# Optimization experiments

Hardware: AMD Instinct MI355X
Metric: run time of the kernel (lower is better)

The kernel has to match this reference:

```python
import jax, jax.numpy as jnp
import numpy as np

HOURS = 168  # 24*7
SU, SL, TU, TL = 100.0, 0.0, 500.0, 0.0  # ex bounds
N, M, L, D, T = 64, 128, 8192, 64, 169  # batch, max_len, l_dim(=u_dim), d_model, t_dim


def setup_inputs() -> dict:
    key = jax.random.key(0)
    ks = jax.random.split(key, 20)
    traj = jax.random.randint(ks[0], (N, M, 3), 1, L)          # [user, loc, time] indices, >=1
    mat1 = jax.random.uniform(ks[1], (N, M, M, 2), jnp.float32) * jnp.asarray([SU, TU], jnp.float32)
    mat2s = jax.random.uniform(ks[2], (L, L), jnp.float32) * SU
    vec = jax.random.uniform(ks[3], (N, M), jnp.float32) * TU
    traj_len = jax.random.randint(ks[4], (N,), 1, M + 1)
    s = 0.02
    emb_t = (jax.random.normal(ks[5], (T, D), jnp.float32) * s).at[0].set(0.0)
    emb_l = (jax.random.normal(ks[6], (L, D), jnp.float32) * s).at[0].set(0.0)
    emb_u = (jax.random.normal(ks[7], (L, D), jnp.float32) * s).at[0].set(0.0)
    emb_su = (jax.random.normal(ks[8], (2, D), jnp.float32) * s).at[0].set(0.0)
    emb_sl = (jax.random.normal(ks[9], (2, D), jnp.float32) * s).at[0].set(0.0)
    emb_tu = (jax.random.normal(ks[10], (2, D), jnp.float32) * s).at[0].set(0.0)
    emb_tl = (jax.random.normal(ks[11], (2, D), jnp.float32) * s).at[0].set(0.0)
    Wq = jax.random.normal(ks[12], (D, D), jnp.float32) * s
    Wk = jax.random.normal(ks[13], (D, D), jnp.float32) * s
    Wv = jax.random.normal(ks[14], (D, D), jnp.float32) * s
    W_out = jax.random.normal(ks[15], (L, D), jnp.float32) * s
    b_out = jnp.zeros((L,), jnp.float32)
    return dict(traj=traj, mat1=mat1, mat2s=mat2s, vec=vec, traj_len=traj_len,
                emb_t=emb_t, emb_l=emb_l, emb_u=emb_u, emb_su=emb_su, emb_sl=emb_sl,
                emb_tu=emb_tu, emb_tl=emb_tl, Wq=Wq, Wk=Wk, Wv=Wv, W_out=W_out, b_out=b_out)


def reference(traj, mat1, mat2s, vec, traj_len, emb_t, emb_l, emb_u,
              emb_su, emb_sl, emb_tu, emb_tl, Wq, Wk, Wv, W_out, b_out):
    # ---- MultiEmbed ----
    time_idx = (traj[:, :, 2] - 1) % HOURS + 1
    joint = emb_t[time_idx] + emb_l[traj[:, :, 1]] + emb_u[traj[:, :, 0]]  # (N,M,D)
    ds, dt = mat1[..., 0], mat1[..., 1]                                    # (N,M,M)
    valid = jnp.arange(M)[None, :] < traj_len[:, None]                     # (N,M)
    mask2 = (valid[:, :, None] & valid[:, None, :]).astype(jnp.int32)      # (N,M,M)
    # delta is only consumed as delta.sum(-1) in SelfAttn; sum over emb dim
    # factors out since vsl/vsu/vtl/vtu are constant over emb -> (N,M,M) only.
    ssl, ssu = emb_sl.sum(-1), emb_su.sum(-1)  # (2,)
    stl, stu = emb_tl.sum(-1), emb_tu.sum(-1)
    delta_sum = ((ssl[mask2] * (SU - ds) + ssu[mask2] * (ds - SL)) / (SU - SL)
                 + (stl[mask2] * (TU - dt) + stu[mask2] * (dt - TL)) / (TU - TL))  # (N,M,M)
    # ---- SelfAttn ----
    q = joint @ Wq.T
    k = joint @ Wk.T
    v = joint @ Wv.T
    scores = jnp.einsum('nmd,npd->nmp', q, k) + delta_sum
    attn = jax.nn.softmax(scores, axis=-1) * mask2.astype(jnp.float32)  # post-softmax ragged mask
    self_attn = jnp.einsum('nmp,npd->nmd', attn, v)                     # (N,M,D)
    # ---- Embed: self_delta (N,M,L,D) consumed only as sum over L in Attn ----
    # mask there equals valid[n,m] for every candidate l, and delta_t = vec for all l,
    # so sum over L collapses to per-(n,m) scalars.
    m1 = valid.astype(jnp.int32)                                  # (N,M)
    E_sl, E_su = emb_sl[m1], emb_su[m1]                           # (N,M,D)
    E_tl, E_tu = emb_tl[m1], emb_tu[m1]
    ds_sum = jnp.where(valid, mat2s.sum(-1)[traj[:, :, 1] - 1], 0.0)  # sum_l delta_s (N,M)
    Lf = jnp.float32(L)
    S_vsl = ds_sum - SL * Lf
    S_vsu = SU * Lf - ds_sum
    S_vtl = (vec - TL) * Lf
    S_vtu = (TU - vec) * Lf
    delta2_sum = ((E_sl * S_vsu[..., None] + E_su * S_vsl[..., None]) / (SU - SL)
                  + (E_tl * S_vtu[..., None] + E_tu * S_vtl[..., None]) / (TU - TL))  # (N,M,D)
    # ---- Attn (training branch: return full logits) ----
    out = (self_attn * delta2_sum) @ W_out.T + b_out  # (N,M,L)
    return out
```

## Files before the change

### kernel.cpp

```cpp
#include <hip/hip_runtime.h>
#include <stdint.h>

#define NB 64
#define MM 128
#define LL 8192
#define DD 64

using f32x4 = __attribute__((ext_vector_type(4))) float;
using bf16x8 = __attribute__((ext_vector_type(8))) short;

__device__ __forceinline__ float bf2f(uint32_t u16) {
    uint32_t v = u16 << 16;
    float f;
    __builtin_memcpy(&f, &v, 4);
    return f;
}
__device__ __forceinline__ uint16_t f2bf(float f) {
    uint32_t x;
    __builtin_memcpy(&x, &f, 4);
    uint32_t r = x + 0x7FFFu + ((x >> 16) & 1u);
    return (uint16_t)(r >> 16);
}
__device__ __forceinline__ float ldf(const void* p, size_t i, bool bf) {
    if (bf) return bf2f(((const uint16_t*)p)[i]);
    return ((const float*)p)[i];
}
__device__ __forceinline__ float4 ldf4(const void* p, size_t i, bool bf) {
    if (bf) {
        uint2 u = *(const uint2*)((const uint16_t*)p + i);
        return make_float4(bf2f(u.x & 0xffffu), bf2f(u.x >> 16), bf2f(u.y & 0xffffu),
                           bf2f(u.y >> 16));
    }
    return *(const float4*)((const float*)p + i);
}
__device__ __forceinline__ float4 ldb4(const uint16_t* p, size_t i) {
    uint2 u = *(const uint2*)(p + i);
    return make_float4(bf2f(u.x & 0xffffu), bf2f(u.x >> 16), bf2f(u.y & 0xffffu), bf2f(u.y >> 16));
}

__global__ __launch_bounds__(256) void k_detect(const uint32_t* __restrict__ p,
                                                int* __restrict__ flag) {
    int t = threadIdx.x;
    int cnt = 0, nz = 0;
    for (int i = t; i < 16384; i += 256) {
        uint32_t w = p[64 + i];
        uint32_t lo = w & 0xffffu;
        if (lo) {
            nz++;
            uint32_t e = (lo >> 7) & 0xffu;
            if (e >= 100 && e <= 130) cnt++;
        }
    }
#pragma unroll
    for (int off = 32; off; off >>= 1) {
        cnt += __shfl_xor(cnt, off, 64);
        nz += __shfl_xor(nz, off, 64);
    }
    __shared__ int sc[4], sn[4];
    if ((t & 63) == 0) {
        sc[t >> 6] = cnt;
        sn[t >> 6] = nz;
    }
    __syncthreads();
    if (t == 0) {
        int C = sc[0] + sc[1] + sc[2] + sc[3];
        int Z = sn[0] + sn[1] + sn[2] + sn[3];
        flag[0] = (2 * C > Z) ? 1 : 0;
    }
}

__global__ __launch_bounds__(256) void k_wprep(const void* __restrict__ Wout,
                                               const int* __restrict__ flag,
                                               uint16_t* __restrict__ whi,
                                               uint16_t* __restrict__ wlo) {
    bool bf = flag[0] != 0;
    int i = blockIdx.x * 256 + threadIdx.x;
    if (bf) {
        uint2 u = *((const uint2*)Wout + i);
        *((uint2*)whi + i) = u;
        *((uint2*)wlo + i) = make_uint2(0u, 0u);
    } else {
        float4 f = *((const float4*)Wout + i);
        uint16_t h0 = f2bf(f.x), h1 = f2bf(f.y), h2 = f2bf(f.z), h3 = f2bf(f.w);
        *((uint2*)whi + i) = make_uint2((uint32_t)h0 | ((uint32_t)h1 << 16),
                                        (uint32_t)h2 | ((uint32_t)h3 << 16));
        uint16_t l0 = f2bf(f.x - bf2f(h0)), l1 = f2bf(f.y - bf2f(h1));
        uint16_t l2 = f2bf(f.z - bf2f(h2)), l3 = f2bf(f.w - bf2f(h3));
        *((uint2*)wlo + i) = make_uint2((uint32_t)l0 | ((uint32_t)l1 << 16),
                                        (uint32_t)l2 | ((uint32_t)l3 << 16));
    }
}

__global__ __launch_bounds__(256) void k_rowsum(const void* __restrict__ mat2s,
                                                const int* __restrict__ flag,
                                                float* __restrict__ rowsum) {
    bool bf = flag[0] != 0;
    int row = blockIdx.x;
    float s = 0.f;
    if (bf) {
        const uint4* p4 = (const uint4*)((const uint16_t*)mat2s + (size_t)row * LL);
#pragma unroll
        for (int c = 0; c < 4; c++) {
            uint4 u = p4[c * 256 + threadIdx.x];
            uint32_t w[4] = {u.x, u.y, u.z, u.w};
#pragma unroll
            for (int q = 0; q < 4; q++) s += bf2f(w[q] & 0xffffu) + bf2f(w[q] >> 16);
        }
    } else {
        const float4* p4 = (const float4*)((const float*)mat2s + (size_t)row * LL);
#pragma unroll
        for (int c = 0; c < 8; c++) {
            float4 v = p4[c * 256 + threadIdx.x];
            s += v.x + v.y + v.z + v.w;
        }
    }
#pragma unroll
    for (int off = 32; off; off >>= 1) s += __shfl_xor(s, off, 64);
    __shared__ float red[4];
    if ((threadIdx.x & 63) == 0) red[threadIdx.x >> 6] = s;
    __syncthreads();
    if (threadIdx.x == 0) rowsum[row] = red[0] + red[1] + red[2] + red[3];
}

__global__ __launch_bounds__(256) void k_qkv(
    const int* __restrict__ traj, const int* __restrict__ flag, const void* __restrict__ emb_t,
    const void* __restrict__ emb_l, const void* __restrict__ emb_u, const void* __restrict__ Wq,
    const void* __restrict__ Wk, const void* __restrict__ Wv, uint16_t* __restrict__ qg,
    uint16_t* __restrict__ kg, uint16_t* __restrict__ vg) {
    bool bf = flag[0] != 0;
    int n = blockIdx.x;
    int t = threadIdx.x;
    __shared__ float joint[MM][DD + 4];
    __shared__ float Wl[DD][DD + 4];
    __shared__ int iu[MM], il[MM], it[MM];

    if (t < MM) {
        iu[t] = traj[((size_t)(n * MM + t)) * 3 + 0];
        il[t] = traj[((size_t)(n * MM + t)) * 3 + 1];
        int tm = traj[((size_t)(n * MM + t)) * 3 + 2];
        it[t] = (tm - 1) % 168 + 1;
    }
    __syncthreads();

    for (int i = t; i < MM * 16; i += 256) {
        int m = i >> 4, c = (i & 15) * 4;
        float4 a = ldf4(emb_t, (size_t)it[m] * DD + c, bf);
        float4 b = ldf4(emb_l, (size_t)il[m] * DD + c, bf);
        float4 d = ldf4(emb_u, (size_t)iu[m] * DD + c, bf);
        joint[m][c]     = a.x + b.x + d.x;
        joint[m][c + 1] = a.y + b.y + d.y;
        joint[m][c + 2] = a.z + b.z + d.z;
        joint[m][c + 3] = a.w + b.w + d.w;
    }

    const void* Ws[3] = {Wq, Wk, Wv};
    uint16_t* outs[3] = {qg, kg, vg};
    int m = t >> 1;
    int dbase = (t & 1) * 32;

    for (int w = 0; w < 3; w++) {
        __syncthreads();
        for (int i = t; i < DD * 16; i += 256) {
            int r = i >> 4, c = (i & 15) * 4;
            float4 a = ldf4(Ws[w], (size_t)r * DD + c, bf);
            Wl[r][c] = a.x;
            Wl[r][c + 1] = a.y;
            Wl[r][c + 2] = a.z;
            Wl[r][c + 3] = a.w;
        }
        __syncthreads();
        float acc[32];
#pragma unroll
        for (int j = 0; j < 32; j++) acc[j] = 0.f;
        for (int kk = 0; kk < DD; kk += 4) {
            float4 j4 = *(const float4*)&joint[m][kk];
#pragma unroll
            for (int j = 0; j < 32; j++) {
                float4 w4 = *(const float4*)&Wl[dbase + j][kk];
                acc[j] += j4.x * w4.x + j4.y * w4.y + j4.z * w4.z + j4.w * w4.w;
            }
        }
        uint32_t* og = (uint32_t*)(outs[w] + ((size_t)(n * MM + m)) * DD + dbase);
#pragma unroll
        for (int j = 0; j < 32; j += 2)
            og[j >> 1] = (uint32_t)f2bf(acc[j]) | ((uint32_t)f2bf(acc[j + 1]) << 16);
    }
}

__global__ __launch_bounds__(256) void k_attn(
    const int* __restrict__ traj, const int* __restrict__ traj_len, const int* __restrict__ flag,
    const void* __restrict__ mat1, const void* __restrict__ vec, const void* __restrict__ emb_su,
    const void* __restrict__ emb_sl, const void* __restrict__ emb_tu,
    const void* __restrict__ emb_tl, const float* __restrict__ rowsum,
    const uint16_t* __restrict__ qg, const uint16_t* __restrict__ kg,
    const uint16_t* __restrict__ vg, uint16_t* __restrict__ hg) {
    bool bf = flag[0] != 0;
    int chunk = blockIdx.x;
    int n = blockIdx.y;
    int t = threadIdx.x;
    __shared__ float kl[MM][DD + 4];
    __shared__ float vl[MM][DD + 4];
    __shared__ float ql[32][DD + 4];
    __shared__ float attn[32][MM + 4];

    int len = traj_len[n];

    for (int i = t; i < MM * 16; i += 256) {
        int r = i >> 4, c = (i & 15) * 4;
        *(float4*)&kl[r][c] = ldb4(kg, ((size_t)(n * MM + r)) * DD + c);
        *(float4*)&vl[r][c] = ldb4(vg, ((size_t)(n * MM + r)) * DD + c);
    }
    for (int i = t; i < 32 * 16; i += 256) {
        int r = i >> 4, c = (i & 15) * 4;
        *(float4*)&ql[r][c] = ldb4(qg, ((size_t)(n * MM + chunk * 32 + r)) * DD + c);
    }
    float ssl = 0.f, ssu = 0.f, stl = 0.f, stu = 0.f;
    for (int d = 0; d < DD; d++) {
        ssl += ldf(emb_sl, DD + d, bf);
        ssu += ldf(emb_su, DD + d, bf);
        stl += ldf(emb_tl, DD + d, bf);
        stu += ldf(emb_tu, DD + d, bf);
    }
    __syncthreads();

    int tx = t & 15, ty = t >> 4;
    float sc[2][8];
#pragma unroll
    for (int i = 0; i < 2; i++)
#pragma unroll
        for (int j = 0; j < 8; j++) sc[i][j] = 0.f;

    for (int kk = 0; kk < DD; kk += 4) {
        float4 q4[2], k4[8];
#pragma unroll
        for (int i = 0; i < 2; i++) q4[i] = *(const float4*)&ql[ty + 16 * i][kk];
#pragma unroll
        for (int j = 0; j < 8; j++) k4[j] = *(const float4*)&kl[tx + 16 * j][kk];
#pragma unroll
        for (int i = 0; i < 2; i++)
#pragma unroll
            for (int j = 0; j < 8; j++)
                sc[i][j] += q4[i].x * k4[j].x + q4[i].y * k4[j].y + q4[i].z * k4[j].z +
                            q4[i].w * k4[j].w;
    }
#pragma unroll
    for (int i = 0; i < 2; i++) {
        int m = chunk * 32 + ty + 16 * i;
        bool vm = m < len;
#pragma unroll
        for (int j = 0; j < 8; j++) {
            int p = tx + 16 * j;
            size_t base = (((size_t)(n * MM + m)) * MM + p) * 2;
            float ds = ldf(mat1, base, bf);
            float dt = ldf(mat1, base + 1, bf);
            bool v2 = vm && (p < len);
            float del = v2 ? ((ssl * (100.f - ds) + ssu * ds) * 0.01f +
                              (stl * (500.f - dt) + stu * dt) * 0.002f)
                           : 0.f;
            sc[i][j] += del;
        }
    }
#pragma unroll
    for (int i = 0; i < 2; i++) {
        float mx = sc[i][0];
#pragma unroll
        for (int j = 1; j < 8; j++) mx = fmaxf(mx, sc[i][j]);
#pragma unroll
        for (int off = 1; off < 16; off <<= 1) mx = fmaxf(mx, __shfl_xor(mx, off, 64));
        float sum = 0.f;
#pragma unroll
        for (int j = 0; j < 8; j++) {
            sc[i][j] = __expf(sc[i][j] - mx);
            sum += sc[i][j];
        }
#pragma unroll
        for (int off = 1; off < 16; off <<= 1) sum += __shfl_xor(sum, off, 64);
        float inv = 1.f / sum;
        int m = chunk * 32 + ty + 16 * i;
        bool vm = m < len;
#pragma unroll
        for (int j = 0; j < 8; j++) {
            int p = tx + 16 * j;
            attn[ty + 16 * i][p] = (vm && p < len) ? sc[i][j] * inv : 0.f;
        }
    }
    __syncthreads();

    float pv[2][4];
#pragma unroll
    for (int i = 0; i < 2; i++)
#pragma unroll
        for (int u = 0; u < 4; u++) pv[i][u] = 0.f;

    for (int pp = 0; pp < MM; pp += 4) {
        float4 a4[2], v4[4];
#pragma unroll
        for (int i = 0; i < 2; i++) a4[i] = *(const float4*)&attn[ty + 16 * i][pp];
#pragma unroll
        for (int u = 0; u < 4; u++) v4[u] = *(const float4*)&vl[pp + u][4 * tx];
#pragma unroll
        for (int i = 0; i < 2; i++) {
            pv[i][0] += a4[i].x * v4[0].x + a4[i].y * v4[1].x + a4[i].z * v4[2].x + a4[i].w * v4[3].x;
            pv[i][1] += a4[i].x * v4[0].y + a4[i].y * v4[1].y + a4[i].z * v4[2].y + a4[i].w * v4[3].y;
            pv[i][2] += a4[i].x * v4[0].z + a4[i].y * v4[1].z + a4[i].z * v4[2].z + a4[i].w * v4[3].z;
            pv[i][3] += a4[i].x * v4[0].w + a4[i].y * v4[1].w + a4[i].z * v4[2].w + a4[i].w * v4[3].w;
        }
    }

#pragma unroll
    for (int i = 0; i < 2; i++) {
        int m = chunk * 32 + ty + 16 * i;
        bool vm = m < len;
        int m1 = vm ? 1 : 0;
        int loc = traj[((size_t)(n * MM + m)) * 3 + 1];
        float rs = vm ? rowsum[loc - 1] : 0.f;
        float vv = ldf(vec, (size_t)(n * MM + m), bf);
        float Svsl = rs;
        float Svsu = 100.f * 8192.f - rs;
        float Svtl = vv * 8192.f;
        float Svtu = (500.f - vv) * 8192.f;
        uint32_t pk[2];
        float hv[4];
#pragma unroll
        for (int u = 0; u < 4; u++) {
            int d = 4 * tx + u;
            float esl = ldf(emb_sl, m1 * DD + d, bf);
            float esu = ldf(emb_su, m1 * DD + d, bf);
            float etl = ldf(emb_tl, m1 * DD + d, bf);
            float etu = ldf(emb_tu, m1 * DD + d, bf);
            float d2 = (esl * Svsu + esu * Svsl) * 0.01f + (etl * Svtu + etu * Svtl) * 0.002f;
            hv[u] = pv[i][u] * d2;
        }
        pk[0] = (uint32_t)f2bf(hv[0]) | ((uint32_t)f2bf(hv[1]) << 16);
        pk[1] = (uint32_t)f2bf(hv[2]) | ((uint32_t)f2bf(hv[3]) << 16);
        *(uint2*)(hg + ((size_t)(n * MM + m)) * DD + 4 * tx) = make_uint2(pk[0], pk[1]);
    }
}

__global__ __launch_bounds__(256, 2) void k_out(const uint16_t* __restrict__ hg,
                                                const int* __restrict__ flag,
                                                const uint16_t* __restrict__ whi,
                                                const uint16_t* __restrict__ wlo,
                                                const void* __restrict__ bout,
                                                void* __restrict__ out) {
    bool bf = flag[0] != 0;
    int ct = blockIdx.x;
    int rt = blockIdx.y;
    int t = threadIdx.x;
    int w = t >> 6, l = t & 63;
    int wr = w >> 1, wc = w & 1;
    int row0 = rt * 128 + wr * 64;
    int col0 = ct * 128 + wc * 64;
    int lr = l & 15;
    int kb = (l >> 4) * 8;

    f32x4 acc[4][4];
#pragma unroll
    for (int i = 0; i < 4; i++)
#pragma unroll
        for (int j = 0; j < 4; j++) acc[i][j] = (f32x4){0.f, 0.f, 0.f, 0.f};

#pragma unroll
    for (int s = 0; s < 2; s++) {
        bf16x8 af[4], bh[4], bl[4];
#pragma unroll
        for (int i = 0; i < 4; i++)
            af[i] = *(const bf16x8*)(hg + (size_t)(row0 + i * 16 + lr) * DD + s * 32 + kb);
#pragma unroll
        for (int j = 0; j < 4; j++) {
            bh[j] = *(const bf16x8*)(whi + (size_t)(col0 + j * 16 + lr) * DD + s * 32 + kb);
            bl[j] = *(const bf16x8*)(wlo + (size_t)(col0 + j * 16 + lr) * DD + s * 32 + kb);
        }
#pragma unroll
        for (int i = 0; i < 4; i++)
#pragma unroll
            for (int j = 0; j < 4; j++) {
                acc[i][j] = __builtin_amdgcn_mfma_f32_16x16x32_bf16(af[i], bh[j], acc[i][j], 0, 0, 0);
                acc[i][j] = __builtin_amdgcn_mfma_f32_16x16x32_bf16(af[i], bl[j], acc[i][j], 0, 0, 0);
            }
    }

    __shared__ float st[4][64][68];
#pragma unroll
    for (int i = 0; i < 4; i++)
#pragma unroll
        for (int j = 0; j < 4; j++)
#pragma unroll
            for (int q = 0; q < 4; q++)
                st[w][i * 16 + (l >> 4) * 4 + q][j * 16 + lr] = acc[i][j][q];

    int cb = col0 + (l & 15) * 4;
    float b0 = ldf(bout, cb + 0, bf), b1 = ldf(bout, cb + 1, bf);
    float b2 = ldf(bout, cb + 2, bf), b3 = ldf(bout, cb + 3, bf);

#pragma unroll
    for (int it = 0; it < 16; it++) {
        int r = it * 4 + (l >> 4);
        float4 v = *(const float4*)&st[w][r][(l & 15) * 4];
        v.x += b0;
        v.y += b1;
        v.z += b2;
        v.w += b3;
        size_t gr = (size_t)(row0 + r) * LL + cb;
        if (bf) {
            uint32_t p0 = (uint32_t)f2bf(v.x) | ((uint32_t)f2bf(v.y) << 16);
            uint32_t p1 = (uint32_t)f2bf(v.z) | ((uint32_t)f2bf(v.w) << 16);
            *(uint2*)((uint16_t*)out + gr) = make_uint2(p0, p1);
        } else {
            *(float4*)((float*)out + gr) = v;
        }
    }
}

extern "C" void kernel_launch(void* const* d_in, const int* in_sizes, int n_in,
                              void* d_out, int out_size, void* d_ws, size_t ws_size,
                              hipStream_t stream) {
    const int* traj     = (const int*)d_in[0];
    const void* mat1    = d_in[1];
    const void* mat2s   = d_in[2];
    const void* vec     = d_in[3];
    const int* traj_len = (const int*)d_in[4];
    const void* emb_t   = d_in[5];
    const void* emb_l   = d_in[6];
    const void* emb_u   = d_in[7];
    const void* emb_su  = d_in[8];
    const void* emb_sl  = d_in[9];
    const void* emb_tu  = d_in[10];
    const void* emb_tl  = d_in[11];
    const void* Wq      = d_in[12];
    const void* Wk      = d_in[13];
    const void* Wv      = d_in[14];
    const void* Wout    = d_in[15];
    const void* bout    = d_in[16];

    char* W = (char*)d_ws;
    int* flag = (int*)W;
    float* rowsum = (float*)(W + 64);
    uint16_t* qg = (uint16_t*)(W + 64 + 32768);
    uint16_t* kg = qg + (size_t)LL * DD;
    uint16_t* vg = kg + (size_t)LL * DD;
    uint16_t* hg = vg + (size_t)LL * DD;
    uint16_t* whi = hg + (size_t)LL * DD;
    uint16_t* wlo = whi + (size_t)LL * DD;

    k_detect<<<dim3(1), dim3(256), 0, stream>>>((const uint32_t*)emb_l, flag);
    k_wprep<<<dim3(512), dim3(256), 0, stream>>>(Wout, flag, whi, wlo);
    k_rowsum<<<dim3(LL), dim3(256), 0, stream>>>(mat2s, flag, rowsum);
    k_qkv<<<dim3(NB), dim3(256), 0, stream>>>(traj, flag, emb_t, emb_l, emb_u, Wq, Wk, Wv, qg, kg,
                                              vg);
    k_attn<<<dim3(4, NB), dim3(256), 0, stream>>>(traj, traj_len, flag, mat1, vec, emb_su, emb_sl,
                                                  emb_tu, emb_tl, rowsum, qg, kg, vg, hg);
    k_out<<<dim3(64, 64), dim3(256), 0, stream>>>(hg, flag, whi, wlo, bout, d_out);
}
```

Baseline: 611.8 us.

## Split QKV projection across blocks, shrink output staging, skip lo-weight MFMA in bf16

The QKV kernel now runs one block per (batch, weight) pair instead of looping over all three weights in one block, which triples parallelism. The output GEMM kernel stages one 16-row slice at a time through a much smaller shared buffer and raises its occupancy hint from 2 to 4 blocks per SM. It also skips the low-part weight MFMAs and their loads when inputs are bf16. The dtype detection scan is shortened to a quarter of the samples, which makes the heuristic less robust.

Result: faster. 570.6 us (-6.7%).

```diff
diff --git a/kernel.cpp b/kernel.cpp
--- a/kernel.cpp
+++ b/kernel.cpp
@@ -42,7 +42,7 @@
                                                 int* __restrict__ flag) {
     int t = threadIdx.x;
     int cnt = 0, nz = 0;
-    for (int i = t; i < 16384; i += 256) {
+    for (int i = t; i < 4096; i += 256) {
         uint32_t w = p[64 + i];
         uint32_t lo = w & 0xffffu;
         if (lo) {
@@ -129,6 +129,7 @@
     uint16_t* __restrict__ kg, uint16_t* __restrict__ vg) {
     bool bf = flag[0] != 0;
     int n = blockIdx.x;
+    int w = blockIdx.y;
     int t = threadIdx.x;
     __shared__ float joint[MM][DD + 4];
     __shared__ float Wl[DD][DD + 4];
@@ -139,6 +140,16 @@
         il[t] = traj[((size_t)(n * MM + t)) * 3 + 1];
         int tm = traj[((size_t)(n * MM + t)) * 3 + 2];
         it[t] = (tm - 1) % 168 + 1;
+    }
+    const void* Ws[3] = {Wq, Wk, Wv};
+    uint16_t* outs[3] = {qg, kg, vg};
+    for (int i = t; i < DD * 16; i += 256) {
+        int r = i >> 4, c = (i & 15) * 4;
+        float4 a = ldf4(Ws[w], (size_t)r * DD + c, bf);
+        Wl[r][c] = a.x;
+        Wl[r][c + 1] = a.y;
+        Wl[r][c + 2] = a.z;
+        Wl[r][c + 3] = a.w;
     }
     __syncthreads();
 
@@ -152,39 +163,25 @@
         joint[m][c + 2] = a.z + b.z + d.z;
         joint[m][c + 3] = a.w + b.w + d.w;
     }
-
-    const void* Ws[3] = {Wq, Wk, Wv};
-    uint16_t* outs[3] = {qg, kg, vg};
+    __syncthreads();
+
     int m = t >> 1;
     int dbase = (t & 1) * 32;
-
-    for (int w = 0; w < 3; w++) {
-        __syncthreads();
-        for (int i = t; i < DD * 16; i += 256) {
-            int r = i >> 4, c = (i & 15) * 4;
-            float4 a = ldf4(Ws[w], (size_t)r * DD + c, bf);
-            Wl[r][c] = a.x;
-            Wl[r][c + 1] = a.y;
-            Wl[r][c + 2] = a.z;
-            Wl[r][c + 3] = a.w;
-        }
-        __syncthreads();
-        float acc[32];
-#pragma unroll
-        for (int j = 0; j < 32; j++) acc[j] = 0.f;
-        for (int kk = 0; kk < DD; kk += 4) {
-            float4 j4 = *(const float4*)&joint[m][kk];
-#pragma unroll
-            for (int j = 0; j < 32; j++) {
-                float4 w4 = *(const float4*)&Wl[dbase + j][kk];
-                acc[j] += j4.x * w4.x + j4.y * w4.y + j4.z * w4.z + j4.w * w4.w;
-            }
-        }
-        uint32_t* og = (uint32_t*)(outs[w] + ((size_t)(n * MM + m)) * DD + dbase);
-#pragma unroll
-        for (int j = 0; j < 32; j += 2)
-            og[j >> 1] = (uint32_t)f2bf(acc[j]) | ((uint32_t)f2bf(acc[j + 1]) << 16);
-    }
+    float acc[32];
+#pragma unroll
+    for (int j = 0; j < 32; j++) acc[j] = 0.f;
+    for (int kk = 0; kk < DD; kk += 4) {
+        float4 j4 = *(const float4*)&joint[m][kk];
+#pragma unroll
+        for (int j = 0; j < 32; j++) {
+            float4 w4 = *(const float4*)&Wl[dbase + j][kk];
+            acc[j] += j4.x * w4.x + j4.y * w4.y + j4.z * w4.z + j4.w * w4.w;
+        }
+    }
+    uint32_t* og = (uint32_t*)(outs[w] + ((size_t)(n * MM + m)) * DD + dbase);
+#pragma unroll
+    for (int j = 0; j < 32; j += 2)
+        og[j >> 1] = (uint32_t)f2bf(acc[j]) | ((uint32_t)f2bf(acc[j + 1]) << 16);
 }
 
 __global__ __launch_bounds__(256) void k_attn(
@@ -337,7 +334,7 @@
     }
 }
 
-__global__ __launch_bounds__(256, 2) void k_out(const uint16_t* __restrict__ hg,
+__global__ __launch_bounds__(256, 4) void k_out(const uint16_t* __restrict__ hg,
                                                 const int* __restrict__ flag,
                                                 const uint16_t* __restrict__ whi,
                                                 const uint16_t* __restrict__ wlo,
@@ -362,52 +359,60 @@
 
 #pragma unroll
     for (int s = 0; s < 2; s++) {
-        bf16x8 af[4], bh[4], bl[4];
+        bf16x8 af[4], bh[4];
 #pragma unroll
         for (int i = 0; i < 4; i++)
             af[i] = *(const bf16x8*)(hg + (size_t)(row0 + i * 16 + lr) * DD + s * 32 + kb);
 #pragma unroll
-        for (int j = 0; j < 4; j++) {
+        for (int j = 0; j < 4; j++)
             bh[j] = *(const bf16x8*)(whi + (size_t)(col0 + j * 16 + lr) * DD + s * 32 + kb);
-            bl[j] = *(const bf16x8*)(wlo + (size_t)(col0 + j * 16 + lr) * DD + s * 32 + kb);
-        }
 #pragma unroll
         for (int i = 0; i < 4; i++)
 #pragma unroll
-            for (int j = 0; j < 4; j++) {
+            for (int j = 0; j < 4; j++)
                 acc[i][j] = __builtin_amdgcn_mfma_f32_16x16x32_bf16(af[i], bh[j], acc[i][j], 0, 0, 0);
-                acc[i][j] = __builtin_amdgcn_mfma_f32_16x16x32_bf16(af[i], bl[j], acc[i][j], 0, 0, 0);
-            }
-    }
-
-    __shared__ float st[4][64][68];
-#pragma unroll
-    for (int i = 0; i < 4; i++)
-#pragma unroll
-        for (int j = 0; j < 4; j++)
-#pragma unroll
-            for (int q = 0; q < 4; q++)
-                st[w][i * 16 + (l >> 4) * 4 + q][j * 16 + lr] = acc[i][j][q];
-
-    int cb = col0 + (l & 15) * 4;
+        if (!bf) {
+            bf16x8 bl[4];
+#pragma unroll
+            for (int j = 0; j < 4; j++)
+                bl[j] = *(const bf16x8*)(wlo + (size_t)(col0 + j * 16 + lr) * DD + s * 32 + kb);
+#pragma unroll
+            for (int i = 0; i < 4; i++)
+#pragma unroll
+                for (int j = 0; j < 4; j++)
+                    acc[i][j] =
+                        __builtin_amdgcn_mfma_f32_16x16x32_bf16(af[i], bl[j], acc[i][j], 0, 0, 0);
+        }
+    }
+
+    int cb = col0 + lr * 4;
     float b0 = ldf(bout, cb + 0, bf), b1 = ldf(bout, cb + 1, bf);
     float b2 = ldf(bout, cb + 2, bf), b3 = ldf(bout, cb + 3, bf);
 
-#pragma unroll
-    for (int it = 0; it < 16; it++) {
-        int r = it * 4 + (l >> 4);
-        float4 v = *(const float4*)&st[w][r][(l & 15) * 4];
-        v.x += b0;
-        v.y += b1;
-        v.z += b2;
-        v.w += b3;
-        size_t gr = (size_t)(row0 + r) * LL + cb;
-        if (bf) {
-            uint32_t p0 = (uint32_t)f2bf(v.x) | ((uint32_t)f2bf(v.y) << 16);
-            uint32_t p1 = (uint32_t)f2bf(v.z) | ((uint32_t)f2bf(v.w) << 16);
-            *(uint2*)((uint16_t*)out + gr) = make_uint2(p0, p1);
-        } else {
-            *(float4*)((float*)out + gr) = v;
+    __shared__ float st[4][16][68];
+#pragma unroll
+    for (int i = 0; i < 4; i++) {
+#pragma unroll
+        for (int j = 0; j < 4; j++)
+#pragma unroll
+            for (int q = 0; q < 4; q++)
+                st[w][(l >> 4) * 4 + q][j * 16 + lr] = acc[i][j][q];
+#pragma unroll
+        for (int it = 0; it < 4; it++) {
+            int r = it * 4 + (l >> 4);
+            float4 v = *(const float4*)&st[w][r][lr * 4];
+            v.x += b0;
+            v.y += b1;
+            v.z += b2;
+            v.w += b3;
+            size_t gr = (size_t)(row0 + i * 16 + r) * LL + cb;
+            if (bf) {
+                uint32_t p0 = (uint32_t)f2bf(v.x) | ((uint32_t)f2bf(v.y) << 16);
+                uint32_t p1 = (uint32_t)f2bf(v.z) | ((uint32_t)f2bf(v.w) << 16);
+                *(uint2*)((uint16_t*)out + gr) = make_uint2(p0, p1);
+            } else {
+                *(float4*)((float*)out + gr) = v;
+            }
         }
     }
 }
@@ -446,8 +451,8 @@
     k_detect<<<dim3(1), dim3(256), 0, stream>>>((const uint32_t*)emb_l, flag);
     k_wprep<<<dim3(512), dim3(256), 0, stream>>>(Wout, flag, whi, wlo);
     k_rowsum<<<dim3(LL), dim3(256), 0, stream>>>(mat2s, flag, rowsum);
-    k_qkv<<<dim3(NB), dim3(256), 0, stream>>>(traj, flag, emb_t, emb_l, emb_u, Wq, Wk, Wv, qg, kg,
-                                              vg);
+    k_qkv<<<dim3(NB, 3), dim3(256), 0, stream>>>(traj, flag, emb_t, emb_l, emb_u, Wq, Wk, Wv, qg,
+                                                 kg, vg);
     k_attn<<<dim3(4, NB), dim3(256), 0, stream>>>(traj, traj_len, flag, mat1, vec, emb_su, emb_sl,
                                                   emb_tu, emb_tl, rowsum, qg, kg, vg, hg);
     k_out<<<dim3(64, 64), dim3(256), 0, stream>>>(hg, flag, whi, wlo, bout, d_out);
```
